# Kernel tuning notes

Hardware: AMD Instinct MI355X
Metric: run time of the kernel (lower is better)

Reference implementation:

```python
import jax, jax.numpy as jnp
import numpy as np

DIM = 256
HEADS = 8
HEAD_DIM = DIM // HEADS
B = 8
HH, WW = 32, 32
N = HH * WW
TABLE = (2 * HH - 1) * (2 * WW - 1)  # 3969
CPB_HID = 512


def _l2norm(t, eps=1e-12):
    # matches torch F.normalize(dim=-1): x / max(||x||, eps)
    n = jnp.sqrt(jnp.sum(t * t, axis=-1, keepdims=True))
    return t / jnp.maximum(n, eps)


def setup_inputs() -> dict:
    key = jax.random.key(0)
    ks = jax.random.split(key, 12)
    x = jax.random.normal(ks[0], (B, N, DIM), dtype=jnp.float32)
    relative_pos_index = jax.random.randint(ks[1], (N, N), 0, TABLE)
    relative_coords_table = jax.random.normal(ks[2], (TABLE, 2), dtype=jnp.float32)
    s = 0.02
    qkv_w = jax.random.normal(ks[3], (3 * DIM, DIM), dtype=jnp.float32) * s
    qkv_b = jnp.zeros((3 * DIM,), dtype=jnp.float32)
    query_embedding = jax.random.normal(ks[4], (HEADS, 1, HEAD_DIM), dtype=jnp.float32) * s
    # temperature init: log(exp(1/0.24) - 1) so softplus(temperature) = 1/0.24
    temperature = jnp.full((HEADS, 1, 1), float(np.log(np.expm1(1.0 / 0.24))), dtype=jnp.float32)
    proj_w = jax.random.normal(ks[5], (DIM, DIM), dtype=jnp.float32) * s
    proj_b = jnp.zeros((DIM,), dtype=jnp.float32)
    cpb_fc1_w = jax.random.normal(ks[6], (CPB_HID, 2), dtype=jnp.float32) * s
    cpb_fc1_b = jnp.zeros((CPB_HID,), dtype=jnp.float32)
    cpb_fc2_w = jax.random.normal(ks[7], (HEADS, CPB_HID), dtype=jnp.float32) * s
    cpb_fc2_b = jnp.zeros((HEADS,), dtype=jnp.float32)
    return dict(x=x, H=HH, W=WW, relative_pos_index=relative_pos_index,
                relative_coords_table=relative_coords_table,
                qkv_w=qkv_w, qkv_b=qkv_b, query_embedding=query_embedding,
                temperature=temperature, proj_w=proj_w, proj_b=proj_b,
                cpb_fc1_w=cpb_fc1_w, cpb_fc1_b=cpb_fc1_b,
                cpb_fc2_w=cpb_fc2_w, cpb_fc2_b=cpb_fc2_b)


def reference(x, H, W, relative_pos_index, relative_coords_table,
              qkv_w, qkv_b, query_embedding, temperature,
              proj_w, proj_b, cpb_fc1_w, cpb_fc1_b, cpb_fc2_w, cpb_fc2_b):
    Bc, Nc, C = x.shape
    seq_length_scale = jnp.asarray(np.log(HH * WW), dtype=x.dtype)  # from init input_resolution
    # qkv projection -> [B, heads, N, head_dim] each
    qkv = (x @ qkv_w.T + qkv_b).reshape(Bc, Nc, 3 * HEADS, HEAD_DIM).transpose(0, 2, 1, 3)
    q, k, v = qkv[:, :HEADS], qkv[:, HEADS:2 * HEADS], qkv[:, 2 * HEADS:]
    # CPB relative position bias: small MLP over coord table, then NxN gather
    h = jax.nn.relu(relative_coords_table @ cpb_fc1_w.T + cpb_fc1_b)  # [T, 512]
    table = (h @ cpb_fc2_w.T + cpb_fc2_b).T                           # [heads, T]
    rel_bias = table[:, relative_pos_index.reshape(-1)].reshape(HEADS, Nc, Nc)
    # cosine attention with learned temperature
    qn = _l2norm(q) + query_embedding[None]                           # [B, heads, N, hd]
    scale = jax.nn.softplus(temperature) * seq_length_scale           # [heads, 1, 1]
    attn = jnp.einsum('bhnd,bhmd->bhnm', qn * scale[None], _l2norm(k)) + rel_bias[None]
    attn = jax.nn.softmax(attn, axis=-1)
    out = jnp.einsum('bhnm,bhmd->bhnd', attn, v).transpose(0, 2, 1, 3).reshape(Bc, Nc, C)
    return out @ proj_w.T + proj_b
```

## Files before the change

kernel.cpp:

```cpp
#include <hip/hip_runtime.h>
#include <hip/hip_bf16.h>
#include <cstddef>
#include <cstdint>

typedef float v4f __attribute__((ext_vector_type(4)));
typedef short v8s __attribute__((ext_vector_type(8)));
typedef _Float16 v8h __attribute__((ext_vector_type(8)));

__device__ __forceinline__ uint32_t fbits(float x){ uint32_t u; __builtin_memcpy(&u,&x,4); return u; }
__device__ __forceinline__ float ffrom(uint32_t u){ float f; __builtin_memcpy(&f,&u,4); return f; }
__device__ __forceinline__ short bf_rh(float x){ return (short)((fbits(x)+0x8000u)>>16); }
__device__ __forceinline__ uint32_t pack_bf_rh(float a, float b){
    uint32_t ua = fbits(a)+0x8000u, ub = fbits(b)+0x8000u;
#if __has_builtin(__builtin_amdgcn_perm)
    return __builtin_amdgcn_perm(ub, ua, 0x07060302u);
#else
    return (ua>>16) | (ub & 0xFFFF0000u);
#endif
}
__device__ __forceinline__ short f2h(float x){ _Float16 h = (_Float16)x; short s; __builtin_memcpy(&s,&h,2); return s; }
__device__ __forceinline__ v8h as_h(v8s s){ v8h h; __builtin_memcpy(&h,&s,16); return h; }
#if __has_builtin(__builtin_amdgcn_exp2f)
#define EXP2(x) __builtin_amdgcn_exp2f(x)
#else
#define EXP2(x) exp2f(x)
#endif

__device__ __forceinline__ void gld16(const void* g, void* l) {
    __builtin_amdgcn_global_load_lds(
        (const __attribute__((address_space(1))) unsigned int*)g,
        (__attribute__((address_space(3))) unsigned int*)l, 16, 0, 0);
}
#define MFMA(a,b,c)  __builtin_amdgcn_mfma_f32_16x16x32_bf16((a),(b),(c),0,0,0)
#define MFMAH(a,b,c) __builtin_amdgcn_mfma_f32_16x16x32_f16((a),(b),(c),0,0,0)

#define LOG2E 1.4426950408889634f

__global__ __launch_bounds__(256)
void cpb_kernel(const float* __restrict__ rct,
                const float* __restrict__ fc1w, const float* __restrict__ fc1b,
                const float* __restrict__ fc2w, const float* __restrict__ fc2b,
                float* __restrict__ table)
{
    __shared__ float s1[1024];
    __shared__ float sb[512];
    __shared__ float s2[4096];
    int tid = threadIdx.x;
    for (int i = tid; i < 1024; i += 256) s1[i] = fc1w[i];
    for (int i = tid; i < 512;  i += 256) sb[i] = fc1b[i];
    for (int i = tid; i < 4096; i += 256) s2[i] = fc2w[i];
    __syncthreads();
    int rl = tid >> 2, jp = tid & 3;
    bool ok = rl < 63;
    int r = blockIdx.x * 63 + rl;
    float c0 = ok ? rct[2*r]   : 0.f;
    float c1 = ok ? rct[2*r+1] : 0.f;
    float a[8] = {0,0,0,0,0,0,0,0};
    int j0 = jp * 128;
    #pragma unroll 4
    for (int j = j0; j < j0 + 128; ++j) {
        float hv = fmaxf(c0*s1[2*j] + c1*s1[2*j+1] + sb[j], 0.0f);
        #pragma unroll
        for (int hh = 0; hh < 8; ++hh) a[hh] += hv * s2[hh*512 + j];
    }
    #pragma unroll
    for (int hh = 0; hh < 8; ++hh) {
        a[hh] += __shfl_xor(a[hh], 1);
        a[hh] += __shfl_xor(a[hh], 2);
    }
    if (ok && jp == 0) {
        #pragma unroll
        for (int hh = 0; hh < 8; ++hh) table[hh*3969 + r] = a[hh] + fc2b[hh];
    }
}

__global__ __launch_bounds__(256)
void bias_mat(const float* __restrict__ tblf, const int* __restrict__ rpi,
              short* __restrict__ biasM)
{
    __shared__ float tb[3969];
    int h   = blockIdx.x >> 6;
    int q16 = blockIdx.x & 63;
    int tid = threadIdx.x;
    int w = tid >> 6, lane = tid & 63, t = lane & 15, quad = lane >> 4;
    for (int i = tid; i < 3969; i += 256) tb[i] = tblf[h*3969 + i] * LOG2E;
    __syncthreads();
    int row0 = q16*16 + quad*4;
    #pragma unroll 1
    for (int kk = 0; kk < 4; ++kk) {
        int kt = w*4 + kk;
        #pragma unroll
        for (int g = 0; g < 4; ++g) {
            float o[4];
            #pragma unroll
            for (int r = 0; r < 4; ++r)
                o[r] = tb[rpi[(size_t)(row0 + r)*1024 + kt*64 + 4*t + g]];
            uint2 pk;
            pk.x = pack_bf_rh(o[0], o[1]);
            pk.y = pack_bf_rh(o[2], o[3]);
            size_t base = ((((size_t)(h*64 + q16)*16 + kt)*4 + g)*64 + lane)*4;
            *(uint2*)(biasM + base) = pk;
        }
    }
}

__global__ __launch_bounds__(256)
void split_kernel(const float* __restrict__ x,  short* __restrict__ xh,
                  const float* __restrict__ wq, short* __restrict__ wqh,
                  const float* __restrict__ wp, short* __restrict__ wph)
{
    int bid = blockIdx.x;
    const float* src; short* dh; int base8;
    if (bid < 1024)      { src = x;  dh = xh;  base8 = bid * 256; }
    else if (bid < 1120) { src = wq; dh = wqh; base8 = (bid-1024) * 256; }
    else                 { src = wp; dh = wph; base8 = (bid-1120) * 256; }
    int e0 = (base8 + (int)threadIdx.x) * 8;
    int m  = e0 >> 8;
    int k  = e0 & 255;
    int kt = k >> 6, c = (k >> 3) & 7;
    float4 f0 = *(const float4*)(src + e0);
    float4 f1 = *(const float4*)(src + e0 + 4);
    float v[8] = {f0.x,f0.y,f0.z,f0.w,f1.x,f1.y,f1.z,f1.w};
    v8s hi;
    #pragma unroll
    for (int j = 0; j < 8; ++j) hi[j] = f2h(v[j]);
    int dst = m*256 + kt*64 + ((c ^ (m & 7)) << 3);
    *(v8s*)&dh[dst] = hi;
}

template<int MODE>
__global__ __launch_bounds__(256)
void gemm_mfma(const short* __restrict__ Ah_g, const short* __restrict__ Wh_g,
               const float* __restrict__ bias, float* __restrict__ C,
               short* __restrict__ qh, short* __restrict__ kh,
               short* __restrict__ vt,
               const float* __restrict__ qe, const float* __restrict__ temp,
               int N)
{
    __shared__ __align__(16) char smem[24576];
    short* Ah = (short*)smem;
    short* Wh = Ah + 128*64;

    int tid  = threadIdx.x;
    int w    = tid >> 6;
    int lane = tid & 63;
    int t    = lane & 15;
    int quad = lane >> 4;
    int m0 = blockIdx.y * 128, n0 = blockIdx.x * 64;
    int Mw = (w >> 1) * 64, Nw = (w & 1) * 32;

    v4f acc[4][2];
    #pragma unroll
    for (int mt = 0; mt < 4; ++mt)
        #pragma unroll
        for (int nt = 0; nt < 2; ++nt) acc[mt][nt] = (v4f){0,0,0,0};

    int lr8 = lane >> 3, lc8 = lane & 7;
    #pragma unroll 1
    for (int kt = 0; kt < 4; ++kt) {
        __syncthreads();
        #pragma unroll
        for (int i = 0; i < 4; ++i) {
            size_t grow = (size_t)(m0 + w*32 + i*8 + lr8) * 256 + kt*64 + lc8*8;
            gld16(Ah_g + grow, Ah + (w*32 + i*8) * 64);
        }
        #pragma unroll
        for (int i = 0; i < 2; ++i) {
            size_t grow = (size_t)(n0 + w*16 + i*8 + lr8) * 256 + kt*64 + lc8*8;
            gld16(Wh_g + grow, Wh + (w*16 + i*8) * 64);
        }
        __syncthreads();
        #pragma unroll
        for (int kk = 0; kk < 2; ++kk) {
            int cp = ((kk*4 + quad) ^ (t & 7)) << 3;
            v8h bh8[2];
            #pragma unroll
            for (int nt = 0; nt < 2; ++nt)
                bh8[nt] = *(const v8h*)&Wh[(Nw + nt*16 + t)*64 + cp];
            #pragma unroll
            for (int mt = 0; mt < 4; ++mt) {
                v8h ah = *(const v8h*)&Ah[(Mw + mt*16 + t)*64 + cp];
                #pragma unroll
                for (int nt = 0; nt < 2; ++nt)
                    acc[mt][nt] = MFMAH(ah, bh8[nt], acc[mt][nt]);
            }
        }
    }

    #pragma unroll
    for (int nt = 0; nt < 2; ++nt) {
        float bv = bias[n0 + Nw + nt*16 + t];
        #pragma unroll
        for (int mt = 0; mt < 4; ++mt)
            #pragma unroll
            for (int r = 0; r < 4; ++r) acc[mt][nt][r] += bv;
    }

    if (MODE == 0) {
        #pragma unroll
        for (int mt = 0; mt < 4; ++mt)
            #pragma unroll
            for (int r = 0; r < 4; ++r) {
                int m = m0 + Mw + mt*16 + quad*4 + r;
                #pragma unroll
                for (int nt = 0; nt < 2; ++nt)
                    C[(size_t)m * N + n0 + Nw + nt*16 + t] = acc[mt][nt][r];
            }
    } else {
        int which = n0 >> 8;
        if (which < 2) {
            int head = ((n0 + Nw) >> 5) & 7;
            float scale = 0.f;
            if (which == 0)
                scale = log1pf(__expf(temp[head])) * 10.0f;
            #pragma unroll
            for (int mt = 0; mt < 4; ++mt)
                #pragma unroll
                for (int r = 0; r < 4; ++r) {
                    float a0 = acc[mt][0][r], a1 = acc[mt][1][r];
                    float s = a0*a0 + a1*a1;
                    s += __shfl_xor(s, 1); s += __shfl_xor(s, 2);
                    s += __shfl_xor(s, 4); s += __shfl_xor(s, 8);
                    float inv = 1.0f / fmaxf(sqrtf(s), 1e-12f);
                    int m = m0 + Mw + mt*16 + quad*4 + r;
                    int b = m >> 10, nrow = m & 1023;
                    if (which == 0) {
                        size_t rowoff = (((size_t)b*8 + head)*1024 + nrow) * 32;
                        #pragma unroll
                        for (int nt = 0; nt < 2; ++nt) {
                            int d = nt*16 + t;
                            float val = (acc[mt][nt][r] * inv + qe[head*32 + d]) * scale;
                            qh[rowoff + d] = f2h(val);
                        }
                    } else {
                        int kk = nrow & 63;
                        int p  = (kk & 3)*16 + (kk >> 2);
                        int prow = (nrow & ~63) | p;
                        int swk = (kk >> 3) & 3;
                        size_t rowoff = (((size_t)b*8 + head)*1024 + prow) * 32;
                        #pragma unroll
                        for (int nt = 0; nt < 2; ++nt) {
                            int d = nt*16 + t;
                            int dpos = (((d >> 3) ^ swk) << 3) | (d & 7);
                            kh[rowoff + dpos] = f2h(acc[mt][nt][r] * inv);
                        }
                    }
                }
        } else {
            __syncthreads();
            short* VT = (short*)smem;
            #pragma unroll
            for (int mt = 0; mt < 4; ++mt)
                #pragma unroll
                for (int nt = 0; nt < 2; ++nt) {
                    int cl = Nw + nt*16 + t;
                    #pragma unroll
                    for (int r = 0; r < 4; ++r) {
                        int rl = Mw + mt*16 + quad*4 + r;
                        VT[cl*136 + rl] = bf_rh(acc[mt][nt][r]);
                    }
                }
            __syncthreads();
            int b = m0 >> 10;
            int keybase = m0 & 1023;
            int headbase = ((n0 - 512) >> 5) & 7;
            int cl = tid >> 2;
            int dim = cl & 31;
            int hd  = headbase + (cl >> 5);
            size_t obase = (((size_t)b*8 + hd)*32 + dim) * 1024 + keybase;
            #pragma unroll
            for (int p = 0; p < 4; ++p) {
                int ci  = (tid & 3) * 4 + p;
                int ktl = ci >> 3, c = ci & 7;
                v8s val = *(const v8s*)&VT[cl*136 + ktl*64 + c*8];
                *(v8s*)&vt[obase + ktl*64 + ((c ^ (dim & 7)) << 3)] = val;
            }
        }
    }
}

__global__ __launch_bounds__(256)
void attn_mfma(const short* __restrict__ qh, const short* __restrict__ kh,
               const short* __restrict__ vt,  const short* __restrict__ biasM,
               short* __restrict__ yh)
{
    __shared__ __align__(16) short Kh_s[2][2048];
    __shared__ __align__(16) short Vt_s[2][2048];
    __shared__ __align__(16) short Ps[4][16][68];

    int bh  = blockIdx.x >> 4;
    int qt  = blockIdx.x & 15;
    int h   = bh & 7;
    int b   = bh >> 3;
    int tid = threadIdx.x;
    int w    = tid >> 6;
    int lane = tid & 63;
    int t    = lane & 15;
    int quad = lane >> 4;

    size_t qoff = ((size_t)bh*1024 + qt*64 + w*16 + t) * 32 + quad*8;
    v8h qf = *(const v8h*)(qh + qoff);

    v4f Oacc[2] = {{0,0,0,0},{0,0,0,0}};
    float lsum[4] = {0,0,0,0};

    size_t kgbase = (size_t)bh * 32768;
    const short* bmb = biasM + ((size_t)(h*64 + qt*4 + w) * 16) * 1024 + lane*4;
    int qrow0 = qt*64 + w*16 + quad*4;
    int swzS = (quad ^ ((t >> 1) & 3)) << 3;
    int lr8 = lane >> 3, lc8 = lane & 7;

    gld16(kh + kgbase + w*512 + lane*8, &Kh_s[0][w*512]);
    gld16(vt + kgbase + (size_t)(w*8 + lr8)*1024 + lc8*8, &Vt_s[0][w*512]);
    uint2 curb[4];
    #pragma unroll
    for (int g = 0; g < 4; ++g) curb[g] = *(const uint2*)(bmb + g*256);

    #pragma unroll 1
    for (int kt = 0; kt < 16; ++kt) {
        int cur = kt & 1;
        __syncthreads();
        uint2 nxtb[4];
        if (kt < 15) {
            int nkt = kt + 1, nb = cur ^ 1;
            gld16(kh + kgbase + (size_t)nkt*2048 + w*512 + lane*8, &Kh_s[nb][w*512]);
            gld16(vt + kgbase + (size_t)(w*8 + lr8)*1024 + nkt*64 + lc8*8, &Vt_s[nb][w*512]);
            const short* bp = bmb + (size_t)nkt*1024;
            #pragma unroll
            for (int g = 0; g < 4; ++g) nxtb[g] = *(const uint2*)(bp + g*256);
        }

        v4f S[4];
        #pragma unroll
        for (int g = 0; g < 4; ++g) {
            v8h kb = *(const v8h*)&Kh_s[cur][(g*16 + t)*32 + swzS];
            v4f c;
            c[0] = ffrom(curb[g].x << 16);
            c[1] = ffrom(curb[g].x & 0xFFFF0000u);
            c[2] = ffrom(curb[g].y << 16);
            c[3] = ffrom(curb[g].y & 0xFFFF0000u);
            S[g] = MFMAH(qf, kb, c);
        }

        #pragma unroll
        for (int r = 0; r < 4; ++r) {
            float p0 = EXP2(S[0][r]);
            float p1 = EXP2(S[1][r]);
            float p2 = EXP2(S[2][r]);
            float p3 = EXP2(S[3][r]);
            lsum[r] += (p0 + p1) + (p2 + p3);
            uint2 pk;
            pk.x = pack_bf_rh(p0, p1);
            pk.y = pack_bf_rh(p2, p3);
            *(uint2*)&Ps[w][quad*4 + r][t*4] = pk;
        }

        #pragma unroll
        for (int ks = 0; ks < 2; ++ks) {
            v8s pf = *(const v8s*)&Ps[w][t][ks*32 + quad*8];
            int vsw = ((ks*4 + quad) ^ (t & 7)) << 3;
            #pragma unroll
            for (int g = 0; g < 2; ++g) {
                v8s vf = *(const v8s*)&Vt_s[cur][(g*16 + t)*64 + vsw];
                Oacc[g] = MFMA(pf, vf, Oacc[g]);
            }
        }
        #pragma unroll
        for (int g = 0; g < 4; ++g) curb[g] = nxtb[g];
    }

    #pragma unroll
    for (int r = 0; r < 4; ++r) {
        float l = lsum[r];
        l += __shfl_xor(l, 1); l += __shfl_xor(l, 2);
        l += __shfl_xor(l, 4); l += __shfl_xor(l, 8);
        float inv = 1.0f / l;
        int qrow = qrow0 + r;
        int m = b*1024 + qrow;
        size_t mbase = (size_t)m * 256;
        int mk = m & 7;
        #pragma unroll
        for (int g = 0; g < 2; ++g) {
            float o = Oacc[g][r] * inv;
            int c = h*4 + g*2 + (t >> 3);
            int chp = ((c ^ mk) << 3) | (t & 7);
            yh[mbase + chp] = f2h(o);
        }
    }
}

extern "C" void kernel_launch(void* const* d_in, const int* in_sizes, int n_in,
                              void* d_out, int out_size, void* d_ws, size_t ws_size,
                              hipStream_t stream)
{
    const float* x     = (const float*)d_in[0];
    const int*   rpi   = (const int*)d_in[3];
    const float* rct   = (const float*)d_in[4];
    const float* qkvw  = (const float*)d_in[5];
    const float* qkvb  = (const float*)d_in[6];
    const float* qe    = (const float*)d_in[7];
    const float* temp  = (const float*)d_in[8];
    const float* projw = (const float*)d_in[9];
    const float* projb = (const float*)d_in[10];
    const float* fc1w  = (const float*)d_in[11];
    const float* fc1b  = (const float*)d_in[12];
    const float* fc2w  = (const float*)d_in[13];
    const float* fc2b  = (const float*)d_in[14];

    char* p = (char*)d_ws;
    float* tblf  = (float*)p;  p += 131072;
    short* xh    = (short*)p;  p += 4194304;
    short* wqh   = (short*)p;  p += 393216;
    short* wph   = (short*)p;  p += 131072;
    short* qh    = (short*)p;  p += 4194304;
    short* kh    = (short*)p;  p += 4194304;
    short* vt    = (short*)p;  p += 4194304;
    short* biasM = (short*)p;  p += 16777216;
    float* out   = (float*)d_out;

    cpb_kernel<<<63, 256, 0, stream>>>(rct, fc1w, fc1b, fc2w, fc2b, tblf);

    bias_mat<<<512, 256, 0, stream>>>(tblf, rpi, biasM);

    split_kernel<<<1152, 256, 0, stream>>>(x, xh, qkvw, wqh, projw, wph);

    dim3 g1(768/64, 8192/128);
    gemm_mfma<1><<<g1, 256, 0, stream>>>(xh, wqh, qkvb, nullptr,
                                         qh, kh, vt, qe, temp, 768);

    attn_mfma<<<1024, 256, 0, stream>>>(qh, kh, vt, biasM, xh);

    dim3 g2(256/64, 8192/128);
    gemm_mfma<0><<<g2, 256, 0, stream>>>(xh, wph, projb, out,
                                         nullptr, nullptr, nullptr,
                                         nullptr, nullptr, 256);
}
```

Baseline: 159.8 us.

## Load K/V fragments directly from global into registers, drop LDS staging

The attention kernel no longer stages K and V tiles in double-buffered shared memory through global_load_lds with a block-wide barrier each step. Each wave now loads its own MFMA K and V fragments straight from global memory into registers, prefetching the next tile alongside the bias. This removes the per-iteration __syncthreads and the LDS traffic. In exchange, the four waves of a block each fetch the same K/V data redundantly from L2 or L1, register pressure rises, and the V loads are strided with 1024-element rows.

```diff
diff --git a/kernel.cpp b/kernel.cpp
--- a/kernel.cpp
+++ b/kernel.cpp
@@ -19,7 +19,6 @@
 #endif
 }
 __device__ __forceinline__ short f2h(float x){ _Float16 h = (_Float16)x; short s; __builtin_memcpy(&s,&h,2); return s; }
-__device__ __forceinline__ v8h as_h(v8s s){ v8h h; __builtin_memcpy(&h,&s,16); return h; }
 #if __has_builtin(__builtin_amdgcn_exp2f)
 #define EXP2(x) __builtin_amdgcn_exp2f(x)
 #else
@@ -284,8 +283,6 @@
                const short* __restrict__ vt,  const short* __restrict__ biasM,
                short* __restrict__ yh)
 {
-    __shared__ __align__(16) short Kh_s[2][2048];
-    __shared__ __align__(16) short Vt_s[2][2048];
     __shared__ __align__(16) short Ps[4][16][68];
 
     int bh  = blockIdx.x >> 4;
@@ -304,42 +301,57 @@
     v4f Oacc[2] = {{0,0,0,0},{0,0,0,0}};
     float lsum[4] = {0,0,0,0};
 
-    size_t kgbase = (size_t)bh * 32768;
+    const short* kbase = kh + (size_t)bh*32768;
+    const short* vbase = vt + (size_t)bh*32768;
     const short* bmb = biasM + ((size_t)(h*64 + qt*4 + w) * 16) * 1024 + lane*4;
     int qrow0 = qt*64 + w*16 + quad*4;
     int swzS = (quad ^ ((t >> 1) & 3)) << 3;
-    int lr8 = lane >> 3, lc8 = lane & 7;
-
-    gld16(kh + kgbase + w*512 + lane*8, &Kh_s[0][w*512]);
-    gld16(vt + kgbase + (size_t)(w*8 + lr8)*1024 + lc8*8, &Vt_s[0][w*512]);
-    uint2 curb[4];
-    #pragma unroll
-    for (int g = 0; g < 4; ++g) curb[g] = *(const uint2*)(bmb + g*256);
-
-    #pragma unroll 1
+
+    int koff[4], voff[2][2];
+    #pragma unroll
+    for (int g = 0; g < 4; ++g) koff[g] = (g*16 + t)*32 + swzS;
+    #pragma unroll
+    for (int ks = 0; ks < 2; ++ks)
+        #pragma unroll
+        for (int g = 0; g < 2; ++g)
+            voff[ks][g] = (g*16 + t)*1024 + (((ks*4 + quad) ^ (t & 7)) << 3);
+
+    v8h Kc[4]; v8s Vc[2][2]; uint2 Bc[4];
+    #pragma unroll
+    for (int g = 0; g < 4; ++g) Kc[g] = *(const v8h*)(kbase + koff[g]);
+    #pragma unroll
+    for (int ks = 0; ks < 2; ++ks)
+        #pragma unroll
+        for (int g = 0; g < 2; ++g) Vc[ks][g] = *(const v8s*)(vbase + voff[ks][g]);
+    #pragma unroll
+    for (int g = 0; g < 4; ++g) Bc[g] = *(const uint2*)(bmb + g*256);
+
+    #pragma unroll 2
     for (int kt = 0; kt < 16; ++kt) {
-        int cur = kt & 1;
-        __syncthreads();
-        uint2 nxtb[4];
+        v8h Kn[4]; v8s Vn[2][2]; uint2 Bn[4];
         if (kt < 15) {
-            int nkt = kt + 1, nb = cur ^ 1;
-            gld16(kh + kgbase + (size_t)nkt*2048 + w*512 + lane*8, &Kh_s[nb][w*512]);
-            gld16(vt + kgbase + (size_t)(w*8 + lr8)*1024 + nkt*64 + lc8*8, &Vt_s[nb][w*512]);
-            const short* bp = bmb + (size_t)nkt*1024;
-            #pragma unroll
-            for (int g = 0; g < 4; ++g) nxtb[g] = *(const uint2*)(bp + g*256);
+            const short* kp = kbase + (kt+1)*2048;
+            const short* vp = vbase + (kt+1)*64;
+            const short* bp = bmb + (size_t)(kt+1)*1024;
+            #pragma unroll
+            for (int g = 0; g < 4; ++g) Kn[g] = *(const v8h*)(kp + koff[g]);
+            #pragma unroll
+            for (int ks = 0; ks < 2; ++ks)
+                #pragma unroll
+                for (int g = 0; g < 2; ++g) Vn[ks][g] = *(const v8s*)(vp + voff[ks][g]);
+            #pragma unroll
+            for (int g = 0; g < 4; ++g) Bn[g] = *(const uint2*)(bp + g*256);
         }
 
         v4f S[4];
         #pragma unroll
         for (int g = 0; g < 4; ++g) {
-            v8h kb = *(const v8h*)&Kh_s[cur][(g*16 + t)*32 + swzS];
             v4f c;
-            c[0] = ffrom(curb[g].x << 16);
-            c[1] = ffrom(curb[g].x & 0xFFFF0000u);
-            c[2] = ffrom(curb[g].y << 16);
-            c[3] = ffrom(curb[g].y & 0xFFFF0000u);
-            S[g] = MFMAH(qf, kb, c);
+            c[0] = ffrom(Bc[g].x << 16);
+            c[1] = ffrom(Bc[g].x & 0xFFFF0000u);
+            c[2] = ffrom(Bc[g].y << 16);
+            c[3] = ffrom(Bc[g].y & 0xFFFF0000u);
+            S[g] = MFMAH(qf, Kc[g], c);
         }
 
         #pragma unroll
@@ -358,15 +370,17 @@
         #pragma unroll
         for (int ks = 0; ks < 2; ++ks) {
             v8s pf = *(const v8s*)&Ps[w][t][ks*32 + quad*8];
-            int vsw = ((ks*4 + quad) ^ (t & 7)) << 3;
-            #pragma unroll
-            for (int g = 0; g < 2; ++g) {
-                v8s vf = *(const v8s*)&Vt_s[cur][(g*16 + t)*64 + vsw];
-                Oacc[g] = MFMA(pf, vf, Oacc[g]);
-            }
-        }
-        #pragma unroll
-        for (int g = 0; g < 4; ++g) curb[g] = nxtb[g];
+            #pragma unroll
+            for (int g = 0; g < 2; ++g)
+                Oacc[g] = MFMA(pf, Vc[ks][g], Oacc[g]);
+        }
+
+        #pragma unroll
+        for (int g = 0; g < 4; ++g) { Kc[g] = Kn[g]; Bc[g] = Bn[g]; }
+        #pragma unroll
+        for (int ks = 0; ks < 2; ++ks)
+            #pragma unroll
+            for (int g = 0; g < 2; ++g) Vc[ks][g] = Vn[ks][g];
     }
 
     #pragma unroll
```

Result: slower. 165.0 us (+3.3%).
